# Optimization experiments

Measured on AMD Instinct MI355X. Metric: run time of the kernel, lower is better.

The kernel has to match this reference:

```python
import jax, jax.numpy as jnp
import numpy as np

LOG2 = 0.6931471824645996  # float32 log(2), shifted-softplus offset

def ssp(v):
    return jax.nn.softplus(v) - LOG2

def setup_inputs() -> dict:
    key = jax.random.key(0)
    ks = jax.random.split(key, 8)
    B, A, N = 4, 512, 128
    n_in = n_factors = n_out = 256
    s_in = 1.0 / np.sqrt(n_in)
    s_f = 1.0 / np.sqrt(n_factors)
    return {
        "x": jax.random.normal(ks[0], (B, A, n_in), dtype=jnp.float32),
        "r_ij": jax.random.uniform(ks[1], (B, A, N), dtype=jnp.float32) * 5.0,
        "pairwise_mask": jnp.ones((B, A, N), dtype=jnp.float32),
        "in2f_w": jax.random.normal(ks[2], (n_in, n_factors), dtype=jnp.float32) * s_in,
        "in2f_b": jnp.zeros((n_factors,), dtype=jnp.float32),
        "f2out_w": jax.random.normal(ks[3], (n_factors, n_out), dtype=jnp.float32) * s_f,
        "f2out_b": jnp.zeros((n_out,), dtype=jnp.float32),
        "fw1": jax.random.normal(ks[4], (1, n_factors), dtype=jnp.float32),
        "fb1": jnp.zeros((n_factors,), dtype=jnp.float32),
        "fw2": jax.random.normal(ks[5], (n_factors, n_factors), dtype=jnp.float32) * s_f,
        "fb2": jnp.zeros((n_factors,), dtype=jnp.float32),
        "neighbors": jax.random.randint(ks[6], (B, A, N), 0, A, dtype=jnp.int64),
    }

def reference(x, r_ij, pairwise_mask, in2f_w, in2f_b, f2out_w, f2out_b,
              fw1, fb1, fw2, fb2, neighbors):
    # f_ij = r_ij.unsqueeze(-1); filter network: Dense+ssp -> Dense
    f_ij = r_ij[..., None]                                  # [B,A,N,1]
    W = ssp(f_ij @ fw1 + fb1) @ fw2 + fb2                   # [B,A,N,F]
    facts = x @ in2f_w + in2f_b                             # [B,A,F]
    B, A, N = neighbors.shape
    F = facts.shape[-1]
    # gather neighbor features along atom axis
    idx = neighbors.reshape(B, A * N)[..., None]            # [B,A*N,1]
    xj = jnp.take_along_axis(facts, idx, axis=1).reshape(B, A, N, F)
    xi = facts[:, :, None, :]                               # [B,A,1,F]
    y = xi * W * xj                                         # [B,A,N,F]
    y = ssp(y @ f2out_w + f2out_b)                          # [B,A,N,n_out]
    return y
```

## Files before the change

### kernel.cpp

```cpp
#include <hip/hip_runtime.h>
#include <hip/hip_bf16.h>
#include <stdint.h>

typedef unsigned short u16;

#define Bdim 4
#define Adim 512
#define Ndim 128
#define Fdim 256
#define BA (Bdim*Adim)

#define HS 264
#define XS 256
#define BK 32
#define BTS 40

typedef __attribute__((ext_vector_type(8))) __bf16 bf16x8;
typedef __attribute__((ext_vector_type(4))) float f32x4;

__device__ __forceinline__ float bf2f(u16 u){
  uint32_t v = ((uint32_t)u) << 16;
  return __builtin_bit_cast(float, v);
}
__device__ __forceinline__ u16 f2bf(float f){
  uint32_t v = __builtin_bit_cast(uint32_t, f);
  v += 0x7fffu + ((v >> 16) & 1u);
  return (u16)(v >> 16);
}
__device__ __forceinline__ float ssp_f(float v){
  float m = fmaxf(v, 0.f);
  float e = __expf(-fabsf(v));
  return m + __logf(1.f + e) - 0.69314718f;
}

__global__ __launch_bounds__(256) void prep_kernel(
    const float* __restrict__ s0, u16* __restrict__ d0,
    const float* __restrict__ s1, u16* __restrict__ d1)
{
  __shared__ float tile[32][33];
  const float* src = blockIdx.y ? s1 : s0;
  u16* dst = blockIdx.y ? d1 : d0;
  int bx = (blockIdx.x & 7) * 32, by = (int)(blockIdx.x >> 3) * 32;
  int tx = threadIdx.x & 31, ty = threadIdx.x >> 5;
  #pragma unroll
  for (int r = 0; r < 4; r++)
    tile[ty + r*8][tx] = src[(size_t)(by + ty + r*8)*Fdim + bx + tx];
  __syncthreads();
  #pragma unroll
  for (int r = 0; r < 4; r++)
    dst[(size_t)(bx + ty + r*8)*Fdim + by + tx] = f2bf(tile[tx][ty + r*8]);
}

__global__ __launch_bounds__(256, 4) void facts_kernel(
    const float* __restrict__ x, const float* __restrict__ w,
    const float* __restrict__ bias, u16* __restrict__ facts)
{
  __shared__ float xs[Fdim];
  const int t = threadIdx.x;
  const int row = blockIdx.x;
  xs[t] = x[(size_t)row*Fdim + t];
  __syncthreads();
  float a0=0.f, a1=0.f, a2=0.f, a3=0.f;
  #pragma unroll 8
  for (int k = 0; k < Fdim; k += 4){
    a0 = fmaf(xs[k  ], w[(size_t)(k  )*Fdim + t], a0);
    a1 = fmaf(xs[k+1], w[(size_t)(k+1)*Fdim + t], a1);
    a2 = fmaf(xs[k+2], w[(size_t)(k+2)*Fdim + t], a2);
    a3 = fmaf(xs[k+3], w[(size_t)(k+3)*Fdim + t], a3);
  }
  facts[(size_t)row*Fdim + t] = f2bf(bias[t] + ((a0+a1)+(a2+a3)));
}

__global__ __launch_bounds__(512, 2) void fused_kernel(
    const float* __restrict__ r_ij, const u16* __restrict__ facts,
    const u16* __restrict__ fw2T, const u16* __restrict__ f2outT,
    const float* __restrict__ fw1, const float* __restrict__ fb1,
    const float* __restrict__ fb2, const float* __restrict__ f2out_b,
    const int* __restrict__ neighbors, float* __restrict__ out)
{
  __shared__ __align__(16) u16 Hs[Ndim*HS];
  __shared__ __align__(16) u16 XJ[Ndim*XS];
  __shared__ __align__(16) u16 BTs[Fdim*BTS];
  __shared__ int   nb_s[Ndim];
  __shared__ float r_s[Ndim];
  __shared__ u16   xi_s[Fdim];
  __shared__ float fw1_s[Fdim], fb1_s[Fdim], fb2_s[Fdim], ob_s[Fdim];

  const int tid = threadIdx.x;
  const int wg  = blockIdx.x;
  const int b   = wg / Adim;

  if (tid < Ndim){
    nb_s[tid] = neighbors[(size_t)wg*Ndim + tid];
    r_s[tid]  = r_ij[(size_t)wg*Ndim + tid];
  }
  if (tid < Fdim){
    xi_s[tid]  = facts[(size_t)wg*Fdim + tid];
    fw1_s[tid] = fw1[tid];
    fb1_s[tid] = fb1[tid];
  } else {
    int t2 = tid - Fdim;
    fb2_s[t2] = fb2[t2];
    ob_s[t2]  = f2out_b[t2];
  }
  __syncthreads();

  #pragma unroll
  for (int i = 0; i < 8; i++){
    int id  = i*512 + tid;
    int row = id >> 5, ch = id & 31;
    const float4* src = (const float4*)(facts + ((size_t)(b*Adim + nb_s[row]))*Fdim + ch*8);
    *(float4*)(XJ + row*XS + ch*8) = *src;
  }
  #pragma unroll 4
  for (int i = 0; i < 64; i++){
    int id  = i*512 + tid;
    int row = id >> 8, f = id & 255;
    Hs[row*HS + f] = f2bf(ssp_f(fmaf(r_s[row], fw1_s[f], fb1_s[f])));
  }

  const int lane = tid & 63;
  const int wid  = tid >> 6;
  const int wrow = (wid >> 2) * 64;
  const int wcol = (wid & 3)  * 64;
  const int l16  = lane & 15;
  const int quad = lane >> 4;

  const int btn = tid >> 1;
  const int bth = (tid & 1) * 16;
  u16* btdst = BTs + btn*BTS + bth;
  const u16* w1src = fw2T   + (size_t)btn*Fdim + bth;
  const u16* w2src = f2outT + (size_t)btn*Fdim + bth;

  float4 pf0 = *(const float4*)(w1src);
  float4 pf1 = *(const float4*)(w1src + 8);

  f32x4 acc[4][4];
  #pragma unroll
  for (int mt = 0; mt < 4; mt++)
    #pragma unroll
    for (int ct = 0; ct < 4; ct++)
      acc[mt][ct] = (f32x4){0.f,0.f,0.f,0.f};

  for (int kk = 0; kk < 8; kk++){
    __syncthreads();
    *(float4*)(btdst)     = pf0;
    *(float4*)(btdst + 8) = pf1;
    if (kk < 7){
      pf0 = *(const float4*)(w1src + (kk+1)*BK);
      pf1 = *(const float4*)(w1src + (kk+1)*BK + 8);
    } else {
      pf0 = *(const float4*)(w2src);
      pf1 = *(const float4*)(w2src + 8);
    }
    __syncthreads();
    bf16x8 af[4], bfr[4];
    #pragma unroll
    for (int mt = 0; mt < 4; mt++)
      af[mt] = *(const bf16x8*)(Hs + (wrow + mt*16 + l16)*HS + kk*BK + quad*8);
    #pragma unroll
    for (int ct = 0; ct < 4; ct++)
      bfr[ct] = *(const bf16x8*)(BTs + (wcol + ct*16 + l16)*BTS + quad*8);
    #pragma unroll
    for (int mt = 0; mt < 4; mt++)
      #pragma unroll
      for (int ct = 0; ct < 4; ct++)
        acc[mt][ct] = __builtin_amdgcn_mfma_f32_16x16x32_bf16(af[mt], bfr[ct], acc[mt][ct], 0, 0, 0);
  }

  __syncthreads();
  #pragma unroll
  for (int ct = 0; ct < 4; ct++){
    int f = wcol + ct*16 + l16;
    float xif  = bf2f(xi_s[f]);
    float fb2v = fb2_s[f];
    #pragma unroll
    for (int mt = 0; mt < 4; mt++){
      #pragma unroll
      for (int i = 0; i < 4; i++){
        int m = wrow + mt*16 + quad*4 + i;
        float wv = acc[mt][ct][i] + fb2v;
        float y  = xif * wv * bf2f(XJ[m*XS + f]);
        Hs[m*HS + f] = f2bf(y);
        acc[mt][ct][i] = 0.f;
      }
    }
  }
  __syncthreads();

  for (int kk = 0; kk < 8; kk++){
    __syncthreads();
    *(float4*)(btdst)     = pf0;
    *(float4*)(btdst + 8) = pf1;
    if (kk < 7){
      pf0 = *(const float4*)(w2src + (kk+1)*BK);
      pf1 = *(const float4*)(w2src + (kk+1)*BK + 8);
    }
    __syncthreads();
    bf16x8 af[4], bfr[4];
    #pragma unroll
    for (int mt = 0; mt < 4; mt++)
      af[mt] = *(const bf16x8*)(Hs + (wrow + mt*16 + l16)*HS + kk*BK + quad*8);
    #pragma unroll
    for (int ct = 0; ct < 4; ct++)
      bfr[ct] = *(const bf16x8*)(BTs + (wcol + ct*16 + l16)*BTS + quad*8);
    #pragma unroll
    for (int mt = 0; mt < 4; mt++)
      #pragma unroll
      for (int ct = 0; ct < 4; ct++)
        acc[mt][ct] = __builtin_amdgcn_mfma_f32_16x16x32_bf16(af[mt], bfr[ct], acc[mt][ct], 0, 0, 0);
  }

  size_t obase = (size_t)wg * (Ndim*Fdim);
  #pragma unroll
  for (int ct = 0; ct < 4; ct++){
    int f = wcol + ct*16 + l16;
    float obv = ob_s[f];
    #pragma unroll
    for (int mt = 0; mt < 4; mt++){
      #pragma unroll
      for (int i = 0; i < 4; i++){
        int m = wrow + mt*16 + quad*4 + i;
        out[obase + (size_t)m*Fdim + f] = ssp_f(acc[mt][ct][i] + obv);
      }
    }
  }
}

extern "C" void kernel_launch(void* const* d_in, const int* in_sizes, int n_in,
                              void* d_out, int out_size, void* d_ws, size_t ws_size,
                              hipStream_t stream)
{
  const float* x        = (const float*)d_in[0];
  const float* r_ij     = (const float*)d_in[1];
  const float* in2f_w   = (const float*)d_in[3];
  const float* in2f_b   = (const float*)d_in[4];
  const float* f2out_w  = (const float*)d_in[5];
  const float* f2out_b  = (const float*)d_in[6];
  const float* fw1      = (const float*)d_in[7];
  const float* fb1      = (const float*)d_in[8];
  const float* fw2      = (const float*)d_in[9];
  const float* fb2      = (const float*)d_in[10];
  const int*   neighbors= (const int*)d_in[11];
  float* out = (float*)d_out;

  u16* facts  = (u16*)d_ws;
  u16* fw2T   = (u16*)((char*)d_ws + (1u<<20));
  u16* f2outT = (u16*)((char*)d_ws + (1u<<20) + (1u<<17));

  prep_kernel<<<dim3(64, 2), 256, 0, stream>>>(fw2, fw2T, f2out_w, f2outT);
  facts_kernel<<<BA, 256, 0, stream>>>(x, in2f_w, in2f_b, facts);
  fused_kernel<<<BA, 512, 0, stream>>>(r_ij, facts, fw2T, f2outT,
                                       fw1, fb1, fb2, f2out_b, neighbors, out);
}
```

Before: 478.5 us.

## Split fused kernel into half-row blocks, stream weights from global via registers, MFMA facts GEMM

The fused kernel now handles 64 neighbor rows per 256-thread block instead of 128 rows per 512 threads, which doubles the grid and roughly halves LDS per block. The B operand fragments come straight from global/L2 into double-buffered registers, removing the shared-memory weight staging and the per-k-step barriers. The facts projection becomes a bf16 MFMA GEMM over a transposed bf16 weight, replacing the scalar FMA loop. The fused kernel also overlaps the neighbor gather loads with the filter computation, vectorises that computation, and writes the output with nontemporal stores. The trade-offs are more repeated global weight reads per output element and bf16 rounding of x.

```diff
diff --git a/kernel.cpp b/kernel.cpp
--- a/kernel.cpp
+++ b/kernel.cpp
@@ -4,19 +4,19 @@
 
 typedef unsigned short u16;
 
-#define Bdim 4
 #define Adim 512
 #define Ndim 128
 #define Fdim 256
-#define BA (Bdim*Adim)
+#define BA 2048
 
 #define HS 264
-#define XS 256
-#define BK 32
-#define BTS 40
+#define XS 264
 
 typedef __attribute__((ext_vector_type(8))) __bf16 bf16x8;
 typedef __attribute__((ext_vector_type(4))) float f32x4;
+
+union pack8 { bf16x8 v; u16 u[8]; };
+union pack4 { uint2 q; u16 u[4]; };
 
 __device__ __forceinline__ float bf2f(u16 u){
   uint32_t v = ((uint32_t)u) << 16;
@@ -35,11 +35,12 @@
 
 __global__ __launch_bounds__(256) void prep_kernel(
     const float* __restrict__ s0, u16* __restrict__ d0,
-    const float* __restrict__ s1, u16* __restrict__ d1)
+    const float* __restrict__ s1, u16* __restrict__ d1,
+    const float* __restrict__ s2, u16* __restrict__ d2)
 {
   __shared__ float tile[32][33];
-  const float* src = blockIdx.y ? s1 : s0;
-  u16* dst = blockIdx.y ? d1 : d0;
+  const float* src = (blockIdx.y == 0) ? s0 : (blockIdx.y == 1 ? s1 : s2);
+  u16* dst = (blockIdx.y == 0) ? d0 : (blockIdx.y == 1 ? d1 : d2);
   int bx = (blockIdx.x & 7) * 32, by = (int)(blockIdx.x >> 3) * 32;
   int tx = threadIdx.x & 31, ty = threadIdx.x >> 5;
   #pragma unroll
@@ -51,89 +52,134 @@
     dst[(size_t)(bx + ty + r*8)*Fdim + by + tx] = f2bf(tile[tx][ty + r*8]);
 }
 
-__global__ __launch_bounds__(256, 4) void facts_kernel(
-    const float* __restrict__ x, const float* __restrict__ w,
+__global__ __launch_bounds__(256, 2) void facts_kernel(
+    const float* __restrict__ x, const u16* __restrict__ wT,
     const float* __restrict__ bias, u16* __restrict__ facts)
 {
-  __shared__ float xs[Fdim];
-  const int t = threadIdx.x;
-  const int row = blockIdx.x;
-  xs[t] = x[(size_t)row*Fdim + t];
-  __syncthreads();
-  float a0=0.f, a1=0.f, a2=0.f, a3=0.f;
-  #pragma unroll 8
-  for (int k = 0; k < Fdim; k += 4){
-    a0 = fmaf(xs[k  ], w[(size_t)(k  )*Fdim + t], a0);
-    a1 = fmaf(xs[k+1], w[(size_t)(k+1)*Fdim + t], a1);
-    a2 = fmaf(xs[k+2], w[(size_t)(k+2)*Fdim + t], a2);
-    a3 = fmaf(xs[k+3], w[(size_t)(k+3)*Fdim + t], a3);
-  }
-  facts[(size_t)row*Fdim + t] = f2bf(bias[t] + ((a0+a1)+(a2+a3)));
-}
-
-__global__ __launch_bounds__(512, 2) void fused_kernel(
+  __shared__ __align__(16) u16 Xs[64*HS];
+  const int tid = threadIdx.x;
+  const int row0 = blockIdx.x * 64;
+
+  #pragma unroll
+  for (int i = 0; i < 16; i++){
+    int id = i*256 + tid;
+    int r = id >> 6, c4 = id & 63;
+    float4 v = *(const float4*)(x + (size_t)(row0 + r)*Fdim + c4*4);
+    pack4 p;
+    p.u[0] = f2bf(v.x); p.u[1] = f2bf(v.y); p.u[2] = f2bf(v.z); p.u[3] = f2bf(v.w);
+    *(uint2*)(Xs + r*HS + c4*4) = p.q;
+  }
+  __syncthreads();
+
+  const int lane = tid & 63, wid = tid >> 6;
+  const int wcol = wid * 64;
+  const int l16 = lane & 15, quad = lane >> 4;
+
+  f32x4 acc[4][4];
+  #pragma unroll
+  for (int mt = 0; mt < 4; mt++)
+    #pragma unroll
+    for (int ct = 0; ct < 4; ct++)
+      acc[mt][ct] = (f32x4){0.f,0.f,0.f,0.f};
+
+  const u16* wbase = wT + (size_t)(wcol + l16)*Fdim + quad*8;
+  bf16x8 bb[2][4];
+  #pragma unroll
+  for (int ct = 0; ct < 4; ct++) bb[0][ct] = *(const bf16x8*)(wbase + ct*16*Fdim);
+
+  for (int kk = 0; kk < 8; kk++){
+    if (kk < 7){
+      #pragma unroll
+      for (int ct = 0; ct < 4; ct++)
+        bb[(kk+1)&1][ct] = *(const bf16x8*)(wbase + ct*16*Fdim + (kk+1)*32);
+    }
+    bf16x8 af[4];
+    #pragma unroll
+    for (int mt = 0; mt < 4; mt++)
+      af[mt] = *(const bf16x8*)(Xs + (mt*16 + l16)*HS + kk*32 + quad*8);
+    #pragma unroll
+    for (int mt = 0; mt < 4; mt++)
+      #pragma unroll
+      for (int ct = 0; ct < 4; ct++)
+        acc[mt][ct] = __builtin_amdgcn_mfma_f32_16x16x32_bf16(af[mt], bb[kk&1][ct], acc[mt][ct], 0, 0, 0);
+  }
+
+  #pragma unroll
+  for (int ct = 0; ct < 4; ct++){
+    int f = wcol + ct*16 + l16;
+    float bv = bias[f];
+    #pragma unroll
+    for (int mt = 0; mt < 4; mt++)
+      #pragma unroll
+      for (int i = 0; i < 4; i++){
+        int m = mt*16 + quad*4 + i;
+        facts[(size_t)(row0 + m)*Fdim + f] = f2bf(acc[mt][ct][i] + bv);
+      }
+  }
+}
+
+__global__ __launch_bounds__(256, 2) void fused_kernel(
     const float* __restrict__ r_ij, const u16* __restrict__ facts,
     const u16* __restrict__ fw2T, const u16* __restrict__ f2outT,
     const float* __restrict__ fw1, const float* __restrict__ fb1,
     const float* __restrict__ fb2, const float* __restrict__ f2out_b,
     const int* __restrict__ neighbors, float* __restrict__ out)
 {
-  __shared__ __align__(16) u16 Hs[Ndim*HS];
-  __shared__ __align__(16) u16 XJ[Ndim*XS];
-  __shared__ __align__(16) u16 BTs[Fdim*BTS];
-  __shared__ int   nb_s[Ndim];
-  __shared__ float r_s[Ndim];
-  __shared__ u16   xi_s[Fdim];
-  __shared__ float fw1_s[Fdim], fb1_s[Fdim], fb2_s[Fdim], ob_s[Fdim];
-
-  const int tid = threadIdx.x;
-  const int wg  = blockIdx.x;
-  const int b   = wg / Adim;
-
-  if (tid < Ndim){
-    nb_s[tid] = neighbors[(size_t)wg*Ndim + tid];
-    r_s[tid]  = r_ij[(size_t)wg*Ndim + tid];
-  }
-  if (tid < Fdim){
-    xi_s[tid]  = facts[(size_t)wg*Fdim + tid];
-    fw1_s[tid] = fw1[tid];
-    fb1_s[tid] = fb1[tid];
-  } else {
-    int t2 = tid - Fdim;
-    fb2_s[t2] = fb2[t2];
-    ob_s[t2]  = f2out_b[t2];
-  }
-  __syncthreads();
-
+  __shared__ __align__(16) u16 Hs[64*HS];
+  __shared__ __align__(16) u16 XJ[64*XS];
+  __shared__ int   nb_s[64];
+  __shared__ float r_s[64];
+
+  const int tid  = threadIdx.x;
+  const int pair = blockIdx.x >> 1;
+  const int half = blockIdx.x & 1;
+  const int rbase = half * 64;
+  const int bbase = (pair / Adim) * Adim;
+
+  if (tid < 64){
+    nb_s[tid] = neighbors[(size_t)pair*Ndim + rbase + tid];
+    r_s[tid]  = r_ij[(size_t)pair*Ndim + rbase + tid];
+  }
+  __syncthreads();
+
+  float4 gx[8];
   #pragma unroll
   for (int i = 0; i < 8; i++){
-    int id  = i*512 + tid;
+    int id = i*256 + tid;
     int row = id >> 5, ch = id & 31;
-    const float4* src = (const float4*)(facts + ((size_t)(b*Adim + nb_s[row]))*Fdim + ch*8);
-    *(float4*)(XJ + row*XS + ch*8) = *src;
-  }
-  #pragma unroll 4
-  for (int i = 0; i < 64; i++){
-    int id  = i*512 + tid;
-    int row = id >> 8, f = id & 255;
-    Hs[row*HS + f] = f2bf(ssp_f(fmaf(r_s[row], fw1_s[f], fb1_s[f])));
-  }
-
-  const int lane = tid & 63;
-  const int wid  = tid >> 6;
-  const int wrow = (wid >> 2) * 64;
-  const int wcol = (wid & 3)  * 64;
-  const int l16  = lane & 15;
-  const int quad = lane >> 4;
-
-  const int btn = tid >> 1;
-  const int bth = (tid & 1) * 16;
-  u16* btdst = BTs + btn*BTS + bth;
-  const u16* w1src = fw2T   + (size_t)btn*Fdim + bth;
-  const u16* w2src = f2outT + (size_t)btn*Fdim + bth;
-
-  float4 pf0 = *(const float4*)(w1src);
-  float4 pf1 = *(const float4*)(w1src + 8);
+    gx[i] = *(const float4*)(facts + ((size_t)(bbase + nb_s[row]))*Fdim + ch*8);
+  }
+
+  #pragma unroll
+  for (int i = 0; i < 8; i++){
+    int id = i*256 + tid;
+    int row = id >> 5, g = id & 31;
+    float rv = r_s[row];
+    float wv[8], cv[8];
+    *(float4*)(wv)   = *(const float4*)(fw1 + g*8);
+    *(float4*)(wv+4) = *(const float4*)(fw1 + g*8 + 4);
+    *(float4*)(cv)   = *(const float4*)(fb1 + g*8);
+    *(float4*)(cv+4) = *(const float4*)(fb1 + g*8 + 4);
+    pack8 p;
+    #pragma unroll
+    for (int j = 0; j < 8; j++)
+      p.u[j] = f2bf(ssp_f(fmaf(rv, wv[j], cv[j])));
+    *(bf16x8*)(Hs + row*HS + g*8) = p.v;
+  }
+
+  #pragma unroll
+  for (int i = 0; i < 8; i++){
+    int id = i*256 + tid;
+    int row = id >> 5, ch = id & 31;
+    *(float4*)(XJ + row*XS + ch*8) = gx[i];
+  }
+
+  const int lane = tid & 63, wid = tid >> 6;
+  const int wcol = wid * 64;
+  const int l16  = lane & 15, quad = lane >> 4;
+
+  const u16* w1base = fw2T   + (size_t)(wcol + l16)*Fdim + quad*8;
+  const u16* w2base = f2outT + (size_t)(wcol + l16)*Fdim + quad*8;
 
   f32x4 acc[4][4];
   #pragma unroll
@@ -142,43 +188,50 @@
     for (int ct = 0; ct < 4; ct++)
       acc[mt][ct] = (f32x4){0.f,0.f,0.f,0.f};
 
+  bf16x8 bb[2][4];
+  #pragma unroll
+  for (int ct = 0; ct < 4; ct++){
+    bb[0][ct] = *(const bf16x8*)(w1base + ct*16*Fdim);
+    bb[1][ct] = *(const bf16x8*)(w1base + ct*16*Fdim + 32);
+  }
+
+  __syncthreads();
+
   for (int kk = 0; kk < 8; kk++){
-    __syncthreads();
-    *(float4*)(btdst)     = pf0;
-    *(float4*)(btdst + 8) = pf1;
-    if (kk < 7){
-      pf0 = *(const float4*)(w1src + (kk+1)*BK);
-      pf1 = *(const float4*)(w1src + (kk+1)*BK + 8);
+    bf16x8 bu[4];
+    #pragma unroll
+    for (int ct = 0; ct < 4; ct++) bu[ct] = bb[kk&1][ct];
+    if (kk < 6){
+      #pragma unroll
+      for (int ct = 0; ct < 4; ct++)
+        bb[kk&1][ct] = *(const bf16x8*)(w1base + ct*16*Fdim + (kk+2)*32);
     } else {
-      pf0 = *(const float4*)(w2src);
-      pf1 = *(const float4*)(w2src + 8);
-    }
-    __syncthreads();
-    bf16x8 af[4], bfr[4];
-    #pragma unroll
-    for (int mt = 0; mt < 4; mt++)
-      af[mt] = *(const bf16x8*)(Hs + (wrow + mt*16 + l16)*HS + kk*BK + quad*8);
-    #pragma unroll
-    for (int ct = 0; ct < 4; ct++)
-      bfr[ct] = *(const bf16x8*)(BTs + (wcol + ct*16 + l16)*BTS + quad*8);
-    #pragma unroll
-    for (int mt = 0; mt < 4; mt++)
-      #pragma unroll
-      for (int ct = 0; ct < 4; ct++)
-        acc[mt][ct] = __builtin_amdgcn_mfma_f32_16x16x32_bf16(af[mt], bfr[ct], acc[mt][ct], 0, 0, 0);
+      #pragma unroll
+      for (int ct = 0; ct < 4; ct++)
+        bb[kk&1][ct] = *(const bf16x8*)(w2base + ct*16*Fdim + (kk-6)*32);
+    }
+    bf16x8 af[4];
+    #pragma unroll
+    for (int mt = 0; mt < 4; mt++)
+      af[mt] = *(const bf16x8*)(Hs + (mt*16 + l16)*HS + kk*32 + quad*8);
+    #pragma unroll
+    for (int mt = 0; mt < 4; mt++)
+      #pragma unroll
+      for (int ct = 0; ct < 4; ct++)
+        acc[mt][ct] = __builtin_amdgcn_mfma_f32_16x16x32_bf16(af[mt], bu[ct], acc[mt][ct], 0, 0, 0);
   }
 
   __syncthreads();
   #pragma unroll
   for (int ct = 0; ct < 4; ct++){
     int f = wcol + ct*16 + l16;
-    float xif  = bf2f(xi_s[f]);
-    float fb2v = fb2_s[f];
+    float xif  = bf2f(facts[(size_t)pair*Fdim + f]);
+    float fb2v = fb2[f];
     #pragma unroll
     for (int mt = 0; mt < 4; mt++){
       #pragma unroll
       for (int i = 0; i < 4; i++){
-        int m = wrow + mt*16 + quad*4 + i;
+        int m = mt*16 + quad*4 + i;
         float wv = acc[mt][ct][i] + fb2v;
         float y  = xif * wv * bf2f(XJ[m*XS + f]);
         Hs[m*HS + f] = f2bf(y);
@@ -189,39 +242,37 @@
   __syncthreads();
 
   for (int kk = 0; kk < 8; kk++){
-    __syncthreads();
-    *(float4*)(btdst)     = pf0;
-    *(float4*)(btdst + 8) = pf1;
-    if (kk < 7){
-      pf0 = *(const float4*)(w2src + (kk+1)*BK);
-      pf1 = *(const float4*)(w2src + (kk+1)*BK + 8);
-    }
-    __syncthreads();
-    bf16x8 af[4], bfr[4];
-    #pragma unroll
-    for (int mt = 0; mt < 4; mt++)
-      af[mt] = *(const bf16x8*)(Hs + (wrow + mt*16 + l16)*HS + kk*BK + quad*8);
-    #pragma unroll
-    for (int ct = 0; ct < 4; ct++)
-      bfr[ct] = *(const bf16x8*)(BTs + (wcol + ct*16 + l16)*BTS + quad*8);
-    #pragma unroll
-    for (int mt = 0; mt < 4; mt++)
-      #pragma unroll
-      for (int ct = 0; ct < 4; ct++)
-        acc[mt][ct] = __builtin_amdgcn_mfma_f32_16x16x32_bf16(af[mt], bfr[ct], acc[mt][ct], 0, 0, 0);
-  }
-
-  size_t obase = (size_t)wg * (Ndim*Fdim);
+    bf16x8 bu[4];
+    #pragma unroll
+    for (int ct = 0; ct < 4; ct++) bu[ct] = bb[kk&1][ct];
+    if (kk < 6){
+      #pragma unroll
+      for (int ct = 0; ct < 4; ct++)
+        bb[kk&1][ct] = *(const bf16x8*)(w2base + ct*16*Fdim + (kk+2)*32);
+    }
+    bf16x8 af[4];
+    #pragma unroll
+    for (int mt = 0; mt < 4; mt++)
+      af[mt] = *(const bf16x8*)(Hs + (mt*16 + l16)*HS + kk*32 + quad*8);
+    #pragma unroll
+    for (int mt = 0; mt < 4; mt++)
+      #pragma unroll
+      for (int ct = 0; ct < 4; ct++)
+        acc[mt][ct] = __builtin_amdgcn_mfma_f32_16x16x32_bf16(af[mt], bu[ct], acc[mt][ct], 0, 0, 0);
+  }
+
+  size_t obase = ((size_t)pair * Ndim + rbase) * Fdim;
   #pragma unroll
   for (int ct = 0; ct < 4; ct++){
     int f = wcol + ct*16 + l16;
-    float obv = ob_s[f];
+    float obv = f2out_b[f];
     #pragma unroll
     for (int mt = 0; mt < 4; mt++){
       #pragma unroll
       for (int i = 0; i < 4; i++){
-        int m = wrow + mt*16 + quad*4 + i;
-        out[obase + (size_t)m*Fdim + f] = ssp_f(acc[mt][ct][i] + obv);
+        int m = mt*16 + quad*4 + i;
+        __builtin_nontemporal_store(ssp_f(acc[mt][ct][i] + obv),
+                                    out + obase + (size_t)m*Fdim + f);
       }
     }
   }
@@ -245,11 +296,12 @@
   float* out = (float*)d_out;
 
   u16* facts  = (u16*)d_ws;
-  u16* fw2T   = (u16*)((char*)d_ws + (1u<<20));
-  u16* f2outT = (u16*)((char*)d_ws + (1u<<20) + (1u<<17));
-
-  prep_kernel<<<dim3(64, 2), 256, 0, stream>>>(fw2, fw2T, f2out_w, f2outT);
-  facts_kernel<<<BA, 256, 0, stream>>>(x, in2f_w, in2f_b, facts);
-  fused_kernel<<<BA, 512, 0, stream>>>(r_ij, facts, fw2T, f2outT,
-                                       fw1, fb1, fb2, f2out_b, neighbors, out);
-}
+  u16* in2fT  = (u16*)((char*)d_ws + (1u<<20));
+  u16* fw2T   = (u16*)((char*)d_ws + (1u<<20) + 1*(1u<<17));
+  u16* f2outT = (u16*)((char*)d_ws + (1u<<20) + 2*(1u<<17));
+
+  prep_kernel<<<dim3(64, 3), 256, 0, stream>>>(in2f_w, in2fT, fw2, fw2T, f2out_w, f2outT);
+  facts_kernel<<<32, 256, 0, stream>>>(x, in2fT, in2f_b, facts);
+  fused_kernel<<<2*BA, 256, 0, stream>>>(r_ij, facts, fw2T, f2outT,
+                                         fw1, fb1, fb2, f2out_b, neighbors, out);
+}
```

Result: slower. 569.1 us (+18.9%).
